# Performance work log

Measured on AMD Instinct MI355X. Metric: run time of the kernel, lower is better.

The kernel has to match this reference:

```python
import jax, jax.numpy as jnp
import numpy as np
import math

B, N, L = 512, 50, 50
D = 128
N_ITEMS = 100000
N_INTENTS = 1024
MAX_LEN = 50
ALPHA = 0.5
STDV = 1.0 / math.sqrt(D)


def _uniform(key, shape):
    return jax.random.uniform(key, shape, dtype=jnp.float32, minval=-STDV, maxval=STDV)


def setup_inputs() -> dict:
    key = jax.random.key(0)
    ks = jax.random.split(key, 24)
    inp = {
        'items': jax.random.randint(ks[0], (B, N), 0, N_ITEMS, dtype=jnp.int64) if jax.config.jax_enable_x64 else jax.random.randint(ks[0], (B, N), 0, N_ITEMS).astype(jnp.int32),
        'A': jax.random.randint(ks[1], (B, N, N), 0, 3, dtype=jnp.int32),
        'inputs': jax.random.randint(ks[2], (B, L), 0, N_ITEMS).astype(jnp.int32),
        'masks': jnp.ones((B, L), dtype=jnp.int32),
        'alias_inputs': jax.random.randint(ks[3], (B, L), 0, N).astype(jnp.int32),
        'item_emb': _uniform(ks[4], (N_ITEMS, D)),
        'intent_emb': _uniform(ks[5], (N_INTENTS, D)),
        'pos_emb': _uniform(ks[6], (MAX_LEN + 1, D)),
        'lq': _uniform(ks[7], (D, D)),
        'lk': _uniform(ks[8], (D, D)),
        'la': _uniform(ks[9], (D,)),
        'lb': _uniform(ks[10], (D,)),
        'la1': _uniform(ks[11], (D,)),
        'la2': _uniform(ks[12], (D,)),
        'lb1': _uniform(ks[13], (D,)),
        'lb2': _uniform(ks[14], (D,)),
        'W1': _uniform(ks[15], (D, D)),
        'b1': _uniform(ks[16], (D,)),
        'W2': _uniform(ks[17], (D, D)),
        'b2': _uniform(ks[18], (D,)),
        'w3': _uniform(ks[19], (D,)),
    }
    inp['items'] = inp['items'].astype(jnp.int32)
    return inp


def _lrelu(x):
    return jnp.where(x >= 0, x, 0.2 * x)


def reference(items, A, inputs, masks, alias_inputs, item_emb, intent_emb, pos_emb,
              lq, lk, la, lb, la1, la2, lb1, lb2, W1, b1, W2, b2, w3):
    n_items, d = item_emb.shape
    n_intents = intent_emb.shape[0]
    # in-place weight L2 row-normalization from torch forward
    item_w = item_emb / jnp.linalg.norm(item_emb, axis=1, keepdims=True)
    intent_w = intent_emb / jnp.linalg.norm(intent_emb, axis=1, keepdims=True)

    # ---- IntentGraph: top-3 sparse routing (softmax is monotonic, topk on logits) ----
    sim = (item_w @ lq) @ (intent_w @ lk).T / jnp.sqrt(jnp.float32(d))  # [Ni, Nc]
    _, idx = jax.lax.top_k(sim, 3)  # [Ni, 3] intent ids per item
    item_idx = jnp.repeat(jnp.arange(n_items), 3)  # [E]
    intent_idx = idx.reshape(-1)                   # [E]

    # sparse softmax over items per intent row, then sparse mm -> new intent emb
    e1 = _lrelu((intent_w[intent_idx] * item_w[item_idx]) @ la)  # [E]
    m1 = jax.ops.segment_max(e1, intent_idx, num_segments=n_intents)
    ex1 = jnp.exp(e1 - m1[intent_idx])
    den1 = jax.ops.segment_sum(ex1, intent_idx, num_segments=n_intents)
    w1e = ex1 / den1[intent_idx]
    intent_new = jax.ops.segment_sum(w1e[:, None] * item_w[item_idx], intent_idx,
                                     num_segments=n_intents)  # [Nc, D]

    # sparse softmax over the 3 intents per item, sparse mm back to items
    nb = intent_new[idx]  # [Ni, 3, D]
    e2 = _lrelu((item_w[:, None, :] * nb) @ lb)  # [Ni, 3]
    w2 = jax.nn.softmax(e2, axis=1)
    item_nei = jnp.einsum('nk,nkd->nd', w2, nb)
    agg = ALPHA * item_w + (1.0 - ALPHA) * item_nei

    # ---- session-level ----
    h_intent = agg[items]   # [B, N, D]
    hi = item_w[items]      # [B, N, D]
    mf = masks.astype(item_w.dtype)  # [B, L]
    hs = (item_w[inputs] * mf[:, :, None]).sum(1) / mf.sum(1, keepdims=True)  # [B, D]

    # ---- LocalGraph: dense NxN attention, two edge types ----
    a1 = _lrelu(jnp.einsum('bid,bjd,d->bij', hi, hi, la1)
                + jnp.einsum('bd,bjd,d->bj', hs, hi, lb1)[:, None, :])
    a2 = _lrelu(jnp.einsum('bid,bjd,d->bij', hi, hi, la2)
                + jnp.einsum('bd,bjd,d->bj', hs, hi, lb2)[:, None, :])
    neg = jnp.float32(-9e15)
    att = jnp.where(A == 1, a1, neg)
    att = jnp.where(A == 2, a2, att)
    att = jax.nn.softmax(att, axis=2)
    h_local = att @ hi  # [B, N, D]

    output = h_local + h_intent + h_local * h_intent
    sessions = jnp.take_along_axis(output, alias_inputs[:, :, None], axis=1)  # [B, L, D]

    # ---- Readout ----
    Ls = alias_inputs.shape[1]
    spe = pos_emb[:Ls][None]  # [1, L, D]
    hir = sessions + spe
    hsr = (hir * mf[:, :, None]).sum(1) / mf.sum(1, keepdims=True)
    q1 = hir @ W1 + b1
    q2 = (hsr @ W2 + b2)[:, None, :]
    al = jax.nn.sigmoid(q1 + q2) @ w3  # [B, L]
    hf = (al[:, :, None] * sessions * mf[:, :, None]).sum(1)  # [B, D]
    pos_n = pos_emb[-1] * (spe * mf[:, :, None]).sum(1) / mf.sum(1, keepdims=True)
    hf = hf + pos_n
    scores = hf @ item_w[1:].T  # [B, n_items-1]
    return scores
```

## Files before the change

kernel.cpp:

```cpp
#include <hip/hip_runtime.h>
#include <math.h>

typedef __attribute__((ext_vector_type(4))) float f32x4;
typedef __attribute__((ext_vector_type(8))) short bf16x8;

static __device__ __forceinline__ unsigned short f2bf(float f) {
  unsigned int u = __float_as_uint(f);
  unsigned int r = (u + 0x7FFFu + ((u >> 16) & 1u)) >> 16;
  return (unsigned short)r;
}
static __device__ __forceinline__ float bf2f(unsigned short h) {
  return __uint_as_float(((unsigned int)h) << 16);
}

#define INS3(vv, cc) do { float _v=(vv); int _c=(cc); \
  if (_v > v2) { if (_v > v1) { v2=v1; c2=c1i; if (_v > v0) { v1=v0; c1i=c0; v0=_v; c0=_c; } \
  else { v1=_v; c1i=_c; } } else { v2=_v; c2=_c; } } } while(0)

#define INS4(vv, cc) do { float _v=(vv); int _c=(cc); \
  if (_v > w3v) { if (_v > w1v) { if (_v > w0v) { w3v=w2v;d3=d2; w2v=w1v;d2=d1; w1v=w0v;d1=d0; w0v=_v;d0=_c; } \
    else { w3v=w2v;d3=d2; w2v=w1v;d2=d1; w1v=_v;d1=_c; } } \
    else { if (_v > w2v) { w3v=w2v;d3=d2; w2v=_v;d2=_c; } else { w3v=_v; d3=_c; } } } } while(0)

__global__ __launch_bounds__(256) void k_norm(const float* __restrict__ in,
                                              float* __restrict__ out, int R) {
  int g = (blockIdx.x * 256 + threadIdx.x) >> 6;
  int lane = threadIdx.x & 63;
  if (g >= R) return;
  float2 v = ((const float2*)(in + (size_t)g * 128))[lane];
  float ss = v.x * v.x + v.y * v.y;
#pragma unroll
  for (int o = 32; o; o >>= 1) ss += __shfl_xor(ss, o, 64);
  float s = 1.0f / sqrtf(ss);
  ((float2*)(out + (size_t)g * 128))[lane] = make_float2(v.x * s, v.y * s);
}

__global__ __launch_bounds__(256) void k_prep_item(const float* __restrict__ in,
                                                   float* __restrict__ item_w,
                                                   unsigned short* __restrict__ itp, int R) {
  int g = (blockIdx.x * 256 + threadIdx.x) >> 6;
  int lane = threadIdx.x & 63;
  if (g >= R) return;
  float2 v = ((const float2*)(in + (size_t)g * 128))[lane];
  float ss = v.x * v.x + v.y * v.y;
#pragma unroll
  for (int o = 32; o; o >>= 1) ss += __shfl_xor(ss, o, 64);
  float s = 1.0f / sqrtf(ss);
  float x = v.x * s, y = v.y * s;
  ((float2*)(item_w + (size_t)g * 128))[lane] = make_float2(x, y);
  unsigned short hx = f2bf(x), hy = f2bf(y);
  unsigned short lx = f2bf(x - bf2f(hx)), ly = f2bf(y - bf2f(hy));
  unsigned short* row = itp + (size_t)g * 384;
  ((ushort2*)row)[lane] = make_ushort2(hx, hy);
  ((ushort2*)(row + 128))[lane] = make_ushort2(hx, hy);
  ((ushort2*)(row + 256))[lane] = make_ushort2(lx, ly);
}

__global__ __launch_bounds__(256) void k_split(const float* __restrict__ in,
                                               unsigned short* __restrict__ outp, int R) {
  int g = (blockIdx.x * 256 + threadIdx.x) >> 6;
  int lane = threadIdx.x & 63;
  if (g >= R) return;
  float2 v = ((const float2*)(in + (size_t)g * 128))[lane];
  unsigned short hx = f2bf(v.x), hy = f2bf(v.y);
  unsigned short lx = f2bf(v.x - bf2f(hx)), ly = f2bf(v.y - bf2f(hy));
  unsigned short* row = outp + (size_t)g * 384;
  ((ushort2*)row)[lane] = make_ushort2(hx, hy);
  ((ushort2*)(row + 128))[lane] = make_ushort2(lx, ly);
  ((ushort2*)(row + 256))[lane] = make_ushort2(hx, hy);
}

__global__ __launch_bounds__(256) void k_t128(const float* __restrict__ in,
                                              float* __restrict__ out) {
  for (int i = threadIdx.x; i < 128 * 128; i += 256) {
    int k = i >> 7, j = i & 127;
    out[j * 128 + k] = in[i];
  }
}

__global__ __launch_bounds__(256) void k_gemm_abt(const float* __restrict__ A,
                                                  const float* __restrict__ B,
                                                  float* __restrict__ C, int M, int N) {
  __shared__ float As[64][132];
  __shared__ float Bs[48][132];
  const int t = threadIdx.x;
  const int m0 = blockIdx.y * 64, n0 = blockIdx.x * 48;
  for (int i = t; i < 64 * 32; i += 256) {
    int r = i >> 5, c4 = (i & 31) << 2;
    float4 v = make_float4(0.f, 0.f, 0.f, 0.f);
    if (m0 + r < M) v = *(const float4*)(A + (size_t)(m0 + r) * 128 + c4);
    *(float4*)&As[r][c4] = v;
  }
  for (int i = t; i < 48 * 32; i += 256) {
    int r = i >> 5, c4 = (i & 31) << 2;
    float4 v = make_float4(0.f, 0.f, 0.f, 0.f);
    if (n0 + r < N) v = *(const float4*)(B + (size_t)(n0 + r) * 128 + c4);
    *(float4*)&Bs[r][c4] = v;
  }
  __syncthreads();
  const int ty = t >> 4, tx = t & 15;
  float acc[4][3];
#pragma unroll
  for (int i = 0; i < 4; i++)
#pragma unroll
    for (int j = 0; j < 3; j++) acc[i][j] = 0.f;
#pragma unroll 4
  for (int k = 0; k < 128; k += 4) {
    float4 a[4], b[3];
#pragma unroll
    for (int i = 0; i < 4; i++) a[i] = *(const float4*)&As[ty + 16 * i][k];
#pragma unroll
    for (int j = 0; j < 3; j++) b[j] = *(const float4*)&Bs[tx + 16 * j][k];
#pragma unroll
    for (int i = 0; i < 4; i++)
#pragma unroll
      for (int j = 0; j < 3; j++) {
        float s = acc[i][j];
        s = fmaf(a[i].x, b[j].x, s);
        s = fmaf(a[i].y, b[j].y, s);
        s = fmaf(a[i].z, b[j].z, s);
        s = fmaf(a[i].w, b[j].w, s);
        acc[i][j] = s;
      }
  }
#pragma unroll
  for (int i = 0; i < 4; i++) {
    int m = m0 + ty + 16 * i;
    if (m >= M) continue;
#pragma unroll
    for (int j = 0; j < 3; j++) {
      int n = n0 + tx + 16 * j;
      if (n < N) C[(size_t)m * N + n] = acc[i][j];
    }
  }
}

template <int MODE>
__global__ __launch_bounds__(256, 2) void k_mfma(const unsigned short* __restrict__ Abase,
                                                 const unsigned short* __restrict__ Bbase,
                                                 float* __restrict__ C, int ldc, int Nc,
                                                 int* __restrict__ pi4, int Mv) {
  __shared__ __align__(16) char lds[32768];
  const int t = threadIdx.x, l = t & 63, w = t >> 6;
  const int wr = w >> 1, wc = w & 1;

  int m0, n0, chunk = 0;
  {
    int g = blockIdx.x;
    int xcd = g & 7, r = g >> 3;
    if (MODE == 0) {
      chunk = r & 7;
      int mt = (r >> 3) * 8 + xcd;
      if (mt >= ((Mv + 127) >> 7)) return;
      m0 = mt << 7;
      n0 = chunk << 7;
    } else {
      int mq = r & 3;
      int nt = (r >> 2) * 8 + xcd;
      if (nt >= ((Nc + 127) >> 7)) return;
      m0 = mq << 7;
      n0 = nt << 7;
    }
  }
  const unsigned short* A = Abase + (size_t)m0 * 384;
  const unsigned short* B = Bbase + (size_t)n0 * 384;

  const int r1 = t >> 2, c1 = t & 3;
  f32x4 acc[4][4];
  {
    f32x4 z = {0.f, 0.f, 0.f, 0.f};
#pragma unroll
    for (int i = 0; i < 4; i++)
#pragma unroll
      for (int j = 0; j < 4; j++) acc[i][j] = z;
  }

  int4 sa0, sa1, sb0, sb1;
  {
    sa0 = *(const int4*)(A + (size_t)r1 * 384 + c1 * 8);
    sa1 = *(const int4*)(A + (size_t)(r1 + 64) * 384 + c1 * 8);
    sb0 = *(const int4*)(B + (size_t)r1 * 384 + c1 * 8);
    sb1 = *(const int4*)(B + (size_t)(r1 + 64) * 384 + c1 * 8);
  }

  for (int kt = 0; kt < 12; ++kt) {
    if (kt) __syncthreads();
    *(int4*)(lds + r1 * 80 + c1 * 16) = sa0;
    *(int4*)(lds + (r1 + 64) * 80 + c1 * 16) = sa1;
    *(int4*)(lds + 10240 + r1 * 80 + c1 * 16) = sb0;
    *(int4*)(lds + 10240 + (r1 + 64) * 80 + c1 * 16) = sb1;
    __syncthreads();
    if (kt < 11) {
      const unsigned short* ka = A + (kt + 1) * 32;
      const unsigned short* kb = B + (kt + 1) * 32;
      sa0 = *(const int4*)(ka + (size_t)r1 * 384 + c1 * 8);
      sa1 = *(const int4*)(ka + (size_t)(r1 + 64) * 384 + c1 * 8);
      sb0 = *(const int4*)(kb + (size_t)r1 * 384 + c1 * 8);
      sb1 = *(const int4*)(kb + (size_t)(r1 + 64) * 384 + c1 * 8);
    }
    bf16x8 af[4], bfr[4];
#pragma unroll
    for (int i = 0; i < 4; i++) {
      int ar = wr * 64 + i * 16 + (l & 15);
      af[i] = *(const bf16x8*)(lds + ar * 80 + (l >> 4) * 16);
      int br = wc * 64 + i * 16 + (l & 15);
      bfr[i] = *(const bf16x8*)(lds + 10240 + br * 80 + (l >> 4) * 16);
    }
#pragma unroll
    for (int i = 0; i < 4; i++)
#pragma unroll
      for (int j = 0; j < 4; j++)
        acc[i][j] = __builtin_amdgcn_mfma_f32_16x16x32_bf16(af[i], bfr[j], acc[i][j], 0, 0, 0);
  }

  if (MODE == 1) {
#pragma unroll
    for (int i = 0; i < 4; i++)
#pragma unroll
      for (int q = 0; q < 4; q++) {
        int m = m0 + wr * 64 + i * 16 + (l >> 4) * 4 + q;
#pragma unroll
        for (int j = 0; j < 4; j++) {
          int n = n0 + wc * 64 + j * 16 + (l & 15);
          if (n < Nc) C[(size_t)m * ldc + n] = acc[i][j][q];
        }
      }
  } else {
    __syncthreads();
    float* sp = (float*)lds;
#pragma unroll
    for (int i = 0; i < 4; i++)
#pragma unroll
      for (int q = 0; q < 4; q++) {
        float va = -3.0e38f, vb = -3.0e38f;
        int ja = 0, jb = 0;
#pragma unroll
        for (int j = 0; j < 4; j++) {
          float v = acc[i][j][q];
          if (v > vb) {
            if (v > va) { vb = va; jb = ja; va = v; ja = j; }
            else { vb = v; jb = j; }
          }
        }
        int row = wr * 64 + i * 16 + (l >> 4) * 4 + q;
        int contrib = wc * 16 + (l & 15);
        sp[(row * 32 + contrib) * 2] =
            __uint_as_float((__float_as_uint(va) & ~3u) | (unsigned)ja);
        sp[(row * 32 + contrib) * 2 + 1] =
            __uint_as_float((__float_as_uint(vb) & ~3u) | (unsigned)jb);
      }
    __syncthreads();
    if (t < 128) {
      int grow = m0 + t;
      if (grow < Mv) {
        float w0v = -3.0e38f, w1v = -3.0e38f, w2v = -3.0e38f, w3v = -3.0e38f;
        int d0 = 0, d1 = 0, d2 = 0, d3 = 0;
        for (int cbt = 0; cbt < 64; cbt++) {
          float v = sp[t * 64 + cbt];
          int contrib = cbt >> 1;
          int j = (int)(__float_as_uint(v) & 3u);
          int col = n0 + (contrib >> 4) * 64 + j * 16 + (contrib & 15);
          INS4(v, col);
        }
        size_t pb = (size_t)grow * 32 + chunk * 4;
        pi4[pb] = d0; pi4[pb + 1] = d1; pi4[pb + 2] = d2; pi4[pb + 3] = d3;
      }
    }
  }
}

__global__ __launch_bounds__(256) void k_rescore(const int* __restrict__ pi4,
                                                 const float* __restrict__ item_w,
                                                 const float* __restrict__ Gt,
                                                 const float* __restrict__ intw,
                                                 const float* __restrict__ la,
                                                 int* __restrict__ idx3,
                                                 float* __restrict__ e1vals,
                                                 int* __restrict__ cnt, int M) {
  int r = (blockIdx.x * 256 + threadIdx.x) >> 6;
  int l = threadIdx.x & 63;
  if (r >= M) return;
  float2 iw = ((const float2*)(item_w + (size_t)r * 128))[l];
  float v0 = -3.0e38f, v1 = -3.0e38f, v2 = -3.0e38f;
  int c0 = 0, c1i = 0, c2 = 0;
  for (int s = 0; s < 32; s++) {
    int c = pi4[(size_t)r * 32 + s];
    float2 g = ((const float2*)(Gt + (size_t)c * 128))[l];
    float d = iw.x * g.x + iw.y * g.y;
#pragma unroll
    for (int o = 32; o; o >>= 1) d += __shfl_xor(d, o, 64);
    INS3(d, c);
  }
  float2 lav = ((const float2*)la)[l];
  float e1v[3];
  int cs[3] = {c0, c1i, c2};
#pragma unroll
  for (int k = 0; k < 3; k++) {
    float2 cw = ((const float2*)(intw + (size_t)cs[k] * 128))[l];
    float d = iw.x * (cw.x * lav.x) + iw.y * (cw.y * lav.y);
#pragma unroll
    for (int o = 32; o; o >>= 1) d += __shfl_xor(d, o, 64);
    e1v[k] = d >= 0.f ? d : 0.2f * d;
  }
  if (l == 0) {
    idx3[r * 3] = c0; idx3[r * 3 + 1] = c1i; idx3[r * 3 + 2] = c2;
    e1vals[r * 3] = e1v[0]; e1vals[r * 3 + 1] = e1v[1]; e1vals[r * 3 + 2] = e1v[2];
    atomicAdd(&cnt[c0], 1); atomicAdd(&cnt[c1i], 1); atomicAdd(&cnt[c2], 1);
  }
}

__global__ __launch_bounds__(1024) void k_scan(const int* __restrict__ cnt,
                                               int* __restrict__ offs,
                                               int* __restrict__ cur) {
  __shared__ int s[1024];
  int t = threadIdx.x;
  int own = cnt[t];
  s[t] = own;
  __syncthreads();
  for (int o = 1; o < 1024; o <<= 1) {
    int v = (t >= o) ? s[t - o] : 0;
    __syncthreads();
    s[t] += v;
    __syncthreads();
  }
  int excl = s[t] - own;
  offs[t] = excl;
  cur[t] = excl;
  if (t == 1023) offs[1024] = s[1023];
}

__global__ void k_scatter(const int* __restrict__ idx3, int* __restrict__ cur,
                          int* __restrict__ edge_id, int E) {
  int e = blockIdx.x * 256 + threadIdx.x;
  if (e < E) {
    int c = idx3[e];
    int pos = atomicAdd(&cur[c], 1);
    edge_id[pos] = e;
  }
}

__global__ __launch_bounds__(512) void k_intent(const float* __restrict__ item_w,
                                                const float* __restrict__ e1vals,
                                                const int* __restrict__ offs,
                                                const int* __restrict__ edge_id,
                                                float* __restrict__ intent_new) {
  int c = blockIdx.x;
  int start = offs[c], end = offs[c + 1];
  int t = threadIdx.x, lane = t & 63, w = t >> 6;
  __shared__ float smx[8], sden[8], sacc[8][128];
  float mx = -3.0e38f;
  for (int e = start + t; e < end; e += 512) mx = fmaxf(mx, e1vals[edge_id[e]]);
#pragma unroll
  for (int o = 32; o; o >>= 1) mx = fmaxf(mx, __shfl_xor(mx, o, 64));
  if (lane == 0) smx[w] = mx;
  __syncthreads();
  mx = smx[0];
#pragma unroll
  for (int i = 1; i < 8; i++) mx = fmaxf(mx, smx[i]);
  float ax = 0.f, ay = 0.f, den = 0.f;
  int e = start + w;
  for (; e + 24 < end; e += 32) {
    int e0 = edge_id[e], e1 = edge_id[e + 8], e2 = edge_id[e + 16], e3 = edge_id[e + 24];
    float2 r0 = ((const float2*)(item_w + (size_t)((unsigned)e0 / 3u) * 128))[lane];
    float2 r1 = ((const float2*)(item_w + (size_t)((unsigned)e1 / 3u) * 128))[lane];
    float2 r2 = ((const float2*)(item_w + (size_t)((unsigned)e2 / 3u) * 128))[lane];
    float2 r3 = ((const float2*)(item_w + (size_t)((unsigned)e3 / 3u) * 128))[lane];
    float w0 = expf(e1vals[e0] - mx), w1 = expf(e1vals[e1] - mx);
    float w2 = expf(e1vals[e2] - mx), w3 = expf(e1vals[e3] - mx);
    ax = fmaf(w0, r0.x, fmaf(w1, r1.x, fmaf(w2, r2.x, fmaf(w3, r3.x, ax))));
    ay = fmaf(w0, r0.y, fmaf(w1, r1.y, fmaf(w2, r2.y, fmaf(w3, r3.y, ay))));
    den += w0 + w1 + w2 + w3;
  }
  for (; e < end; e += 8) {
    int e0 = edge_id[e];
    float2 r0 = ((const float2*)(item_w + (size_t)((unsigned)e0 / 3u) * 128))[lane];
    float w0 = expf(e1vals[e0] - mx);
    ax = fmaf(w0, r0.x, ax);
    ay = fmaf(w0, r0.y, ay);
    den += w0;
  }
  sacc[w][2 * lane] = ax;
  sacc[w][2 * lane + 1] = ay;
  if (lane == 0) sden[w] = den;
  __syncthreads();
  if (t < 128) {
    float s = 0.f;
#pragma unroll
    for (int i = 0; i < 8; i++) s += sacc[i][t];
    float dt = 0.f;
#pragma unroll
    for (int i = 0; i < 8; i++) dt += sden[i];
    float inv = dt > 0.f ? 1.f / dt : 0.f;
    intent_new[(size_t)c * 128 + t] = s * inv;
  }
}

__global__ __launch_bounds__(256) void k_hintent(const int* __restrict__ items,
                                                 const float* __restrict__ item_w,
                                                 const int* __restrict__ idx3,
                                                 const float* __restrict__ intent_new,
                                                 const float* __restrict__ lb,
                                                 float* __restrict__ h_intent, int total) {
  int g = (blockIdx.x * 256 + threadIdx.x) >> 6;
  int lane = threadIdx.x & 63;
  if (g >= total) return;
  int it = items[g];
  float2 iw = ((const float2*)(item_w + (size_t)it * 128))[lane];
  float2 lbv = ((const float2*)lb)[lane];
  float e2[3];
  float2 nb[3];
#pragma unroll
  for (int k = 0; k < 3; k++) {
    int c = idx3[(size_t)it * 3 + k];
    nb[k] = ((const float2*)(intent_new + (size_t)c * 128))[lane];
    float d = iw.x * nb[k].x * lbv.x + iw.y * nb[k].y * lbv.y;
#pragma unroll
    for (int o = 32; o; o >>= 1) d += __shfl_xor(d, o, 64);
    e2[k] = d >= 0.f ? d : 0.2f * d;
  }
  float m = fmaxf(fmaxf(e2[0], e2[1]), e2[2]);
  float x0 = expf(e2[0] - m), x1 = expf(e2[1] - m), x2 = expf(e2[2] - m);
  float inv = 1.f / (x0 + x1 + x2);
  float nx = (x0 * nb[0].x + x1 * nb[1].x + x2 * nb[2].x) * inv;
  float ny = (x0 * nb[0].y + x1 * nb[1].y + x2 * nb[2].y) * inv;
  ((float2*)(h_intent + (size_t)g * 128))[lane] =
      make_float2(0.5f * iw.x + 0.5f * nx, 0.5f * iw.y + 0.5f * ny);
}

__global__ __launch_bounds__(512) void k_session(
    const int* __restrict__ items, const int* __restrict__ Aadj,
    const int* __restrict__ inputs, const int* __restrict__ masks,
    const int* __restrict__ alias_inp, const float* __restrict__ item_w,
    const float* __restrict__ pos_emb, const float* __restrict__ la1,
    const float* __restrict__ la2, const float* __restrict__ lb1,
    const float* __restrict__ lb2, const float* __restrict__ W1,
    const float* __restrict__ b1, const float* __restrict__ W2,
    const float* __restrict__ b2, const float* __restrict__ w3,
    const float* __restrict__ h_intent, float* __restrict__ hf_out) {
  const int b = blockIdx.x;
  const int t = threadIdx.x;
  const int lane = t & 63, w = t >> 6;
  __shared__ float hi[50][128];
  __shared__ float outb[6400];
  __shared__ float attb[2504];
  __shared__ float hsb[128], hsrb[128], q2b[128];
  __shared__ float cj1v[50], cj2v[50], alb[50];
  __shared__ float4 lab[128];

  float* hiT = outb;
  float* att = attb;
  float* tmp4 = attb;
  float* wred = attb + 512;

  float mfs = 0.f;
  for (int l = 0; l < 50; l++) mfs += (float)masks[b * 50 + l];

  for (int i = t; i < 50 * 32; i += 512) {
    int r = i >> 5, c4 = (i & 31) << 2;
    int it = items[b * 50 + r];
    *(float4*)&hi[r][c4] = *(const float4*)(item_w + (size_t)it * 128 + c4);
  }
  if (t < 128) lab[t] = make_float4(la1[t], la2[t], lb1[t], lb2[t]);
  {
    int d = t & 127, g = t >> 7;
    float acc = 0.f;
    for (int l = g; l < 50; l += 4) {
      float m = (float)masks[b * 50 + l];
      int row = inputs[b * 50 + l];
      acc += m * item_w[(size_t)row * 128 + d];
    }
    tmp4[g * 128 + d] = acc;
  }
  __syncthreads();
  if (t < 128) hsb[t] = (tmp4[t] + tmp4[128 + t] + tmp4[256 + t] + tmp4[384 + t]) / mfs;
  for (int i = t; i < 6400; i += 512) {
    int r = i >> 7, d = i & 127;
    hiT[d * 50 + r] = hi[r][d];
  }
  __syncthreads();
  if (w == 0) {
    int jc = lane < 50 ? lane : 49;
    float s1 = 0.f, s2 = 0.f;
#pragma unroll 8
    for (int d = 0; d < 128; d++) {
      float xj = hiT[d * 50 + jc];
      float4 c = lab[d];
      float hv = hsb[d];
      s1 = fmaf(hv * c.z, xj, s1);
      s2 = fmaf(hv * c.w, xj, s2);
    }
    if (lane < 50) { cj1v[lane] = s1; cj2v[lane] = s2; }
  }
  __syncthreads();
  for (int i = w; i < 50; i += 8) {
    int jc = lane < 50 ? lane : 49;
    float s1 = 0.f, s2 = 0.f;
#pragma unroll 8
    for (int d = 0; d < 128; d++) {
      float xi = hiT[d * 50 + i];
      float4 c = lab[d];
      float xj = hiT[d * 50 + jc];
      s1 = fmaf(xi * c.x, xj, s1);
      s2 = fmaf(xi * c.y, xj, s2);
    }
    float v = -9e15f;
    if (lane < 50) {
      int a = Aadj[((size_t)b * 50 + i) * 50 + lane];
      if (a == 1) { float x = s1 + cj1v[lane]; v = x >= 0.f ? x : 0.2f * x; }
      else if (a == 2) { float x = s2 + cj2v[lane]; v = x >= 0.f ? x : 0.2f * x; }
    }
    float mx = v;
#pragma unroll
    for (int o = 32; o; o >>= 1) mx = fmaxf(mx, __shfl_xor(mx, o, 64));
    float ex = lane < 50 ? expf(v - mx) : 0.f;
    float sm = ex;
#pragma unroll
    for (int o = 32; o; o >>= 1) sm += __shfl_xor(sm, o, 64);
    if (lane < 50) att[i * 50 + lane] = ex / sm;
  }
  __syncthreads();
  for (int i = w; i < 50; i += 8) {
    float ax = 0.f, ay = 0.f;
    for (int j = 0; j < 50; j++) {
      float a = att[i * 50 + j];
      float2 xj = *(const float2*)&hi[j][2 * lane];
      ax = fmaf(a, xj.x, ax);
      ay = fmaf(a, xj.y, ay);
    }
    float2 hv = ((const float2*)(h_intent + ((size_t)b * 50 + i) * 128))[lane];
    *(float2*)&outb[i * 128 + 2 * lane] =
        make_float2(ax + hv.x + ax * hv.x, ay + hv.y + ay * hv.y);
  }
  __syncthreads();
  for (int i = t; i < 50 * 64; i += 512) {
    int r = i >> 6, c2 = (i & 63) << 1;
    int a = alias_inp[b * 50 + r];
    *(float2*)&hi[r][c2] = *(const float2*)&outb[a * 128 + c2];
  }
  __syncthreads();
  for (int i = t; i < 50 * 64; i += 512) {
    int r = i >> 6, c2 = (i & 63) << 1;
    float2 s = *(const float2*)&hi[r][c2];
    float2 pp = *(const float2*)(pos_emb + (size_t)r * 128 + c2);
    *(float2*)&outb[r * 128 + c2] = make_float2(s.x + pp.x, s.y + pp.y);
  }
  __syncthreads();
  {
    int d = t & 127, g = t >> 7;
    float acc = 0.f;
    for (int l = g; l < 50; l += 4) acc += (float)masks[b * 50 + l] * outb[l * 128 + d];
    tmp4[g * 128 + d] = acc;
  }
  __syncthreads();
  if (t < 128) hsrb[t] = (tmp4[t] + tmp4[128 + t] + tmp4[256 + t] + tmp4[384 + t]) / mfs;
  __syncthreads();
  {
    int d = t & 127, g = t >> 7;
    float acc = 0.f;
    for (int k = g * 32; k < g * 32 + 32; k++)
      acc = fmaf(hsrb[k], W2[(size_t)k * 128 + d], acc);
    tmp4[g * 128 + d] = acc;
  }
  __syncthreads();
  if (t < 128) q2b[t] = b2[t] + tmp4[t] + tmp4[128 + t] + tmp4[256 + t] + tmp4[384 + t];
  __syncthreads();
  {
    int d = t & 127, g = t >> 7;
    float accq[13];
#pragma unroll
    for (int jj = 0; jj < 13; jj++) accq[jj] = b1[d];
    for (int k = 0; k < 128; k += 2) {
      float w1a = W1[(size_t)k * 128 + d];
      float w1b = W1[(size_t)(k + 1) * 128 + d];
#pragma unroll
      for (int jj = 0; jj < 13; jj++) {
        int l = g + 4 * jj;
        int le = l < 50 ? l : 0;
        float2 hv = *(const float2*)&outb[le * 128 + k];
        accq[jj] = fmaf(hv.x, w1a, accq[jj]);
        accq[jj] = fmaf(hv.y, w1b, accq[jj]);
      }
    }
    float w3v = w3[d], q2v = q2b[d];
#pragma unroll
    for (int jj = 0; jj < 13; jj++) {
      float s = 1.f / (1.f + expf(-(accq[jj] + q2v))) * w3v;
#pragma unroll
      for (int o = 32; o; o >>= 1) s += __shfl_xor(s, o, 64);
      if (lane == 0) wred[w * 13 + jj] = s;
    }
  }
  __syncthreads();
  if (t < 50) {
    int g = t & 3, jj = t >> 2;
    alb[t] = wred[(2 * g) * 13 + jj] + wred[(2 * g + 1) * 13 + jj];
  }
  __syncthreads();
  if (t < 128) {
    int d = t;
    float acc = 0.f, pacc = 0.f;
    for (int l = 0; l < 50; l++) {
      float m = (float)masks[b * 50 + l];
      acc += alb[l] * hi[l][d] * m;
      pacc += pos_emb[(size_t)l * 128 + d] * m;
    }
    hf_out[(size_t)b * 128 + d] = acc + pos_emb[50 * 128 + d] * (pacc / mfs);
  }
}

extern "C" void kernel_launch(void* const* d_in, const int* in_sizes, int n_in,
                              void* d_out, int out_size, void* d_ws, size_t ws_size,
                              hipStream_t stream) {
  const int* items = (const int*)d_in[0];
  const int* Aadj = (const int*)d_in[1];
  const int* inputs = (const int*)d_in[2];
  const int* masks = (const int*)d_in[3];
  const int* alias = (const int*)d_in[4];
  const float* item_emb = (const float*)d_in[5];
  const float* intent_emb = (const float*)d_in[6];
  const float* pos_emb = (const float*)d_in[7];
  const float* lq = (const float*)d_in[8];
  const float* lk = (const float*)d_in[9];
  const float* la = (const float*)d_in[10];
  const float* lb = (const float*)d_in[11];
  const float* la1 = (const float*)d_in[12];
  const float* la2 = (const float*)d_in[13];
  const float* lb1 = (const float*)d_in[14];
  const float* lb2 = (const float*)d_in[15];
  const float* W1 = (const float*)d_in[16];
  const float* b1 = (const float*)d_in[17];
  const float* W2 = (const float*)d_in[18];
  const float* b2 = (const float*)d_in[19];
  const float* w3 = (const float*)d_in[20];
  float* out = (float*)d_out;

  char* p = (char*)d_ws;
  auto alloc = [&](size_t bytes) {
    char* r = p;
    p += (bytes + 511) & ~(size_t)511;
    return r;
  };
  float* item_w = (float*)alloc(100000ull * 128 * 4);
  unsigned short* itp = (unsigned short*)alloc(100104ull * 384 * 2);
  unsigned short* gtp = (unsigned short*)alloc(1024ull * 384 * 2);
  float* intw = (float*)alloc(1024ull * 128 * 4);
  float* CK = (float*)alloc(1024ull * 128 * 4);
  float* Gt = (float*)alloc(1024ull * 128 * 4);
  float* lkT = (float*)alloc(128 * 128 * 4);
  int* idx3 = (int*)alloc(300000ull * 4);
  float* e1vals = (float*)alloc(300000ull * 4);
  int* cnt = (int*)alloc(1024 * 4);
  int* offs = (int*)alloc(1025 * 4);
  int* cur = (int*)alloc(1024 * 4);
  int* edge_id = (int*)alloc(300000ull * 4);
  char* big = alloc(13107200);
  int* pi4 = (int*)big;
  float* h_int = (float*)big;
  float* hf = (float*)alloc(512 * 128 * 4);
  float* hfp_f = (float*)alloc(512ull * 384 * 2);
  unsigned short* hfp = (unsigned short*)hfp_f;

  k_prep_item<<<25000, 256, 0, stream>>>(item_emb, item_w, itp, 100000);
  k_norm<<<256, 256, 0, stream>>>(intent_emb, intw, 1024);
  k_t128<<<1, 256, 0, stream>>>(lk, lkT);
  k_gemm_abt<<<dim3(3, 16), 256, 0, stream>>>(intw, lkT, CK, 1024, 128);
  k_gemm_abt<<<dim3(3, 16), 256, 0, stream>>>(CK, lq, Gt, 1024, 128);
  k_split<<<256, 256, 0, stream>>>(Gt, gtp, 1024);

  hipMemsetAsync(cnt, 0, 1024 * 4, stream);
  k_mfma<0><<<6272, 256, 0, stream>>>(itp, gtp, nullptr, 0, 1024, pi4, 100000);
  k_rescore<<<25000, 256, 0, stream>>>(pi4, item_w, Gt, intw, la, idx3, e1vals, cnt, 100000);

  k_scan<<<1, 1024, 0, stream>>>(cnt, offs, cur);
  k_scatter<<<(300000 + 255) / 256, 256, 0, stream>>>(idx3, cur, edge_id, 300000);
  k_intent<<<1024, 512, 0, stream>>>(item_w, e1vals, offs, edge_id, (float*)CK);
  k_hintent<<<6400, 256, 0, stream>>>(items, item_w, idx3, (float*)CK, lb, h_int, 25600);
  k_session<<<512, 512, 0, stream>>>(items, Aadj, inputs, masks, alias, item_w, pos_emb,
                                     la1, la2, lb1, lb2, W1, b1, W2, b2, w3, h_int, hf);
  k_split<<<128, 256, 0, stream>>>(hf, hfp, 512);
  k_mfma<1><<<3136, 256, 0, stream>>>(hfp, itp + 384, out, 99999, 99999, nullptr, 512);
}
```

Baseline: 1.133 ms.

## Restructure rescore kernel to one thread per candidate with shared-memory top-3

The rescore kernel used to give each item row a full 64-lane wavefront and loop over 32 candidates, doing a shuffle reduction for every dot product. Now each block handles 8 rows, and each thread computes one candidate's full 128-dim dot product serially. The item row is staged in shared memory, and one thread per row does the top-3 selection from shared memory. This removes the serial candidate loop and the shuffle reductions, but each thread now reads a whole Gt row uncoalesced, and the top-3 pass is serialized on 8 threads.

```diff
diff --git a/kernel.cpp b/kernel.cpp
--- a/kernel.cpp
+++ b/kernel.cpp
@@ -277,35 +277,75 @@
                                                  int* __restrict__ idx3,
                                                  float* __restrict__ e1vals,
                                                  int* __restrict__ cnt, int M) {
-  int r = (blockIdx.x * 256 + threadIdx.x) >> 6;
-  int l = threadIdx.x & 63;
-  if (r >= M) return;
-  float2 iw = ((const float2*)(item_w + (size_t)r * 128))[l];
-  float v0 = -3.0e38f, v1 = -3.0e38f, v2 = -3.0e38f;
-  int c0 = 0, c1i = 0, c2 = 0;
-  for (int s = 0; s < 32; s++) {
-    int c = pi4[(size_t)r * 32 + s];
-    float2 g = ((const float2*)(Gt + (size_t)c * 128))[l];
-    float d = iw.x * g.x + iw.y * g.y;
-#pragma unroll
-    for (int o = 32; o; o >>= 1) d += __shfl_xor(d, o, 64);
-    INS3(d, c);
-  }
-  float2 lav = ((const float2*)la)[l];
-  float e1v[3];
-  int cs[3] = {c0, c1i, c2};
-#pragma unroll
-  for (int k = 0; k < 3; k++) {
-    float2 cw = ((const float2*)(intw + (size_t)cs[k] * 128))[l];
-    float d = iw.x * (cw.x * lav.x) + iw.y * (cw.y * lav.y);
-#pragma unroll
-    for (int o = 32; o; o >>= 1) d += __shfl_xor(d, o, 64);
-    e1v[k] = d >= 0.f ? d : 0.2f * d;
-  }
-  if (l == 0) {
-    idx3[r * 3] = c0; idx3[r * 3 + 1] = c1i; idx3[r * 3 + 2] = c2;
-    e1vals[r * 3] = e1v[0]; e1vals[r * 3 + 1] = e1v[1]; e1vals[r * 3 + 2] = e1v[2];
-    atomicAdd(&cnt[c0], 1); atomicAdd(&cnt[c1i], 1); atomicAdd(&cnt[c2], 1);
+  __shared__ float iwS[8][128];
+  __shared__ float laS[128];
+  __shared__ float sval[8][32];
+  __shared__ int scol[8][32];
+  __shared__ int sc3[8][3];
+  const int t = threadIdx.x;
+  const int rbase = blockIdx.x * 8;
+  {
+    int row = t >> 5, c4 = (t & 31) << 2;
+    int gr = rbase + row;
+    float4 v = make_float4(0.f, 0.f, 0.f, 0.f);
+    if (gr < M) v = *(const float4*)(item_w + (size_t)gr * 128 + c4);
+    *(float4*)&iwS[row][c4] = v;
+  }
+  if (t < 32) ((float4*)laS)[t] = ((const float4*)la)[t];
+  __syncthreads();
+  const int row = t >> 5, s = t & 31;
+  const int gr = rbase + row;
+  float val = -3.0e38f;
+  int col = 0;
+  if (gr < M) {
+    col = pi4[(size_t)gr * 32 + s];
+    const float4* g4 = (const float4*)(Gt + (size_t)col * 128);
+    float a0 = 0.f, a1 = 0.f, a2 = 0.f, a3 = 0.f;
+#pragma unroll
+    for (int d4 = 0; d4 < 32; d4 += 4) {
+      float4 x0 = *(const float4*)&iwS[row][d4 * 4];
+      float4 y0 = g4[d4];
+      float4 x1 = *(const float4*)&iwS[row][d4 * 4 + 4];
+      float4 y1 = g4[d4 + 1];
+      float4 x2 = *(const float4*)&iwS[row][d4 * 4 + 8];
+      float4 y2 = g4[d4 + 2];
+      float4 x3 = *(const float4*)&iwS[row][d4 * 4 + 12];
+      float4 y3 = g4[d4 + 3];
+      a0 = fmaf(x0.x, y0.x, fmaf(x0.y, y0.y, fmaf(x0.z, y0.z, fmaf(x0.w, y0.w, a0))));
+      a1 = fmaf(x1.x, y1.x, fmaf(x1.y, y1.y, fmaf(x1.z, y1.z, fmaf(x1.w, y1.w, a1))));
+      a2 = fmaf(x2.x, y2.x, fmaf(x2.y, y2.y, fmaf(x2.z, y2.z, fmaf(x2.w, y2.w, a2))));
+      a3 = fmaf(x3.x, y3.x, fmaf(x3.y, y3.y, fmaf(x3.z, y3.z, fmaf(x3.w, y3.w, a3))));
+    }
+    val = (a0 + a1) + (a2 + a3);
+  }
+  sval[row][s] = val;
+  scol[row][s] = col;
+  __syncthreads();
+  if (t < 8) {
+    int grr = rbase + t;
+    if (grr < M) {
+      float v0 = -3.0e38f, v1 = -3.0e38f, v2 = -3.0e38f;
+      int c0 = 0, c1i = 0, c2 = 0;
+      for (int s2 = 0; s2 < 32; s2++) INS3(sval[t][s2], scol[t][s2]);
+      idx3[grr * 3] = c0; idx3[grr * 3 + 1] = c1i; idx3[grr * 3 + 2] = c2;
+      sc3[t][0] = c0; sc3[t][1] = c1i; sc3[t][2] = c2;
+      atomicAdd(&cnt[c0], 1); atomicAdd(&cnt[c1i], 1); atomicAdd(&cnt[c2], 1);
+    }
+  }
+  __syncthreads();
+  if (gr < M && s < 3) {
+    int c = sc3[row][s];
+    const float4* cw = (const float4*)(intw + (size_t)c * 128);
+    float acc = 0.f;
+#pragma unroll
+    for (int d4 = 0; d4 < 32; d4++) {
+      float4 a = *(const float4*)&iwS[row][d4 * 4];
+      float4 lv = *(const float4*)&laS[d4 * 4];
+      float4 b = cw[d4];
+      acc = fmaf(a.x * lv.x, b.x,
+            fmaf(a.y * lv.y, b.y, fmaf(a.z * lv.z, b.z, fmaf(a.w * lv.w, b.w, acc))));
+    }
+    e1vals[gr * 3 + s] = acc >= 0.f ? acc : 0.2f * acc;
   }
 }
 
@@ -669,7 +709,7 @@
 
   hipMemsetAsync(cnt, 0, 1024 * 4, stream);
   k_mfma<0><<<6272, 256, 0, stream>>>(itp, gtp, nullptr, 0, 1024, pi4, 100000);
-  k_rescore<<<25000, 256, 0, stream>>>(pi4, item_w, Gt, intw, la, idx3, e1vals, cnt, 100000);
+  k_rescore<<<12500, 256, 0, stream>>>(pi4, item_w, Gt, intw, la, idx3, e1vals, cnt, 100000);
 
   k_scan<<<1, 1024, 0, stream>>>(cnt, offs, cur);
   k_scatter<<<(300000 + 255) / 256, 256, 0, stream>>>(idx3, cur, edge_id, 300000);
```

Measured after the change: 1.097 ms. 3.2% less time.
